# Optimization experiments

Measured on AMD Instinct MI355X. Metric: run time of the kernel, lower is better.

Reference implementation:

```python
import jax, jax.numpy as jnp
import numpy as np

LEAKY_SLOPE = 0.2  # PyG GATConv default negative_slope
EPS = 1e-16


def _gat_layer(h_in, src, dst, W, a_src, a_dst, b, concat):
    # h_in: [N, Fin]; src/dst: [Etot] (self-loops included); W: [Fin, H*C]
    N = h_in.shape[0]
    H, C = a_src.shape
    h = (h_in @ W).reshape(N, H, C)                       # [N,H,C]
    al_s = jnp.sum(h * a_src, axis=-1)                    # [N,H]
    al_d = jnp.sum(h * a_dst, axis=-1)                    # [N,H]
    e = jax.nn.leaky_relu(al_s[src] + al_d[dst], LEAKY_SLOPE)  # [E,H]
    emax = jax.ops.segment_max(e, dst, num_segments=N)    # segment softmax over dst
    p = jnp.exp(e - emax[dst])
    denom = jax.ops.segment_sum(p, dst, num_segments=N)
    alpha = p / (denom[dst] + EPS)                        # [E,H]
    out = jax.ops.segment_sum(h[src] * alpha[:, :, None], dst, num_segments=N)  # [N,H,C]
    out = out.reshape(N, H * C) if concat else out.mean(axis=1)
    return out + b


def setup_inputs() -> dict:
    key = jax.random.key(0)
    ks = jax.random.split(key, 16)
    N, E, Fin, Hd, Hh = 10000, 320000, 256, 128, 4

    def glorot(k, shape, fan_in):
        return jax.random.normal(k, shape, dtype=jnp.float32) * (1.0 / np.sqrt(fan_in))

    inp = {
        "x": jax.random.normal(ks[0], (N, Fin), dtype=jnp.float32),
        "edge_index": jax.random.randint(ks[1], (2, E), 0, N, dtype=jnp.int32),
        # conv1: Fin -> Hd x Hh heads, concat
        "W1": glorot(ks[2], (Fin, Hh * Hd), Fin),
        "a1_src": glorot(ks[3], (Hh, Hd), Hd),
        "a1_dst": glorot(ks[4], (Hh, Hd), Hd),
        "b1": jnp.zeros((Hh * Hd,), jnp.float32),
        # conv2: Hh*Hd -> Hd x Hh heads, concat
        "W2": glorot(ks[5], (Hh * Hd, Hh * Hd), Hh * Hd),
        "a2_src": glorot(ks[6], (Hh, Hd), Hd),
        "a2_dst": glorot(ks[7], (Hh, Hd), Hd),
        "b2": jnp.zeros((Hh * Hd,), jnp.float32),
        # conv3: Hh*Hd -> Hd, 1 head, concat=False (mean)
        "W3": glorot(ks[8], (Hh * Hd, Hd), Hh * Hd),
        "a3_src": glorot(ks[9], (1, Hd), Hd),
        "a3_dst": glorot(ks[10], (1, Hd), Hd),
        "b3": jnp.zeros((Hd,), jnp.float32),
        # classifier: Hd -> Hd//2 -> 2
        "Wc1": glorot(ks[11], (Hd, Hd // 2), Hd),
        "bc1": jnp.zeros((Hd // 2,), jnp.float32),
        "Wc2": glorot(ks[12], (Hd // 2, 2), Hd // 2),
        "bc2": jnp.zeros((2,), jnp.float32),
    }
    return inp


def reference(x, edge_index, W1, a1_src, a1_dst, b1, W2, a2_src, a2_dst, b2,
              W3, a3_src, a3_dst, b3, Wc1, bc1, Wc2, bc2):
    N = x.shape[0]
    loops = jnp.arange(N, dtype=edge_index.dtype)
    src = jnp.concatenate([edge_index[0], loops])  # PyG adds self-loops
    dst = jnp.concatenate([edge_index[1], loops])

    h = jax.nn.elu(_gat_layer(x, src, dst, W1, a1_src, a1_dst, b1, concat=True))
    h = jax.nn.elu(_gat_layer(h, src, dst, W2, a2_src, a2_dst, b2, concat=True))
    embeddings = _gat_layer(h, src, dst, W3, a3_src, a3_dst, b3, concat=False)  # [N, 128]
    out = jax.nn.relu(embeddings @ Wc1 + bc1) @ Wc2 + bc2  # [N, 2]
    return out, embeddings
```

## Files before the change

kernel.cpp:

```cpp
#include <hip/hip_runtime.h>
#include <cstddef>

#define LEAKY 0.2f
#define EPS_DEN 1e-16f

typedef short bf8_t __attribute__((ext_vector_type(8)));
typedef float f4_t __attribute__((ext_vector_type(4)));
typedef unsigned short us4_t __attribute__((ext_vector_type(4)));

__device__ __forceinline__ unsigned short f2bf(float f) {
    unsigned u = __float_as_uint(f);
    unsigned r = (u + 0x7fffu + ((u >> 16) & 1u)) >> 16;
    return (unsigned short)r;
}
__device__ __forceinline__ float bf2f(unsigned short h) {
    return __uint_as_float(((unsigned)h) << 16);
}

__global__ void hist_kernel(const int* __restrict__ dst, int* __restrict__ counts, int E) {
    int i = blockIdx.x * blockDim.x + threadIdx.x;
    if (i < E) atomicAdd(&counts[dst[i]], 1);
}

__global__ void scan1_kernel(int* __restrict__ cnt, int* __restrict__ bsum, int N) {
    __shared__ int s[256];
    int t = threadIdx.x;
    int i = blockIdx.x * 256 + t;
    int v = (i < N) ? cnt[i] : 0;
    s[t] = v;
    __syncthreads();
#pragma unroll
    for (int st = 1; st < 256; st <<= 1) {
        int add = (t >= st) ? s[t - st] : 0;
        __syncthreads();
        s[t] += add;
        __syncthreads();
    }
    if (i < N) cnt[i] = s[t] - v;
    if (t == 255) bsum[blockIdx.x] = s[255];
}

__global__ void scan2_kernel(int* __restrict__ bsum, int* __restrict__ offs, int NB, int N) {
    int t = threadIdx.x;
    int v = (t < NB) ? bsum[t] : 0;
    int inc = v;
#pragma unroll
    for (int off = 1; off < 64; off <<= 1) {
        int u = __shfl_up(inc, off);
        if (t >= off) inc += u;
    }
    if (t < NB) bsum[t] = inc - v;
    if (t == 63) offs[N] = inc;
}

__global__ void scan3_kernel(int* __restrict__ cnt, const int* __restrict__ bsum,
                             int* __restrict__ offs, int N) {
    int i = blockIdx.x * 256 + threadIdx.x;
    if (i < N) {
        int o = cnt[i] + bsum[blockIdx.x];
        offs[i] = o;
        cnt[i] = o;
    }
}

__global__ void scatter_kernel(const int* __restrict__ src, const int* __restrict__ dst,
                               int* __restrict__ cursor, int* __restrict__ csrc, int E) {
    int i = blockIdx.x * blockDim.x + threadIdx.x;
    if (i < E) {
        int d = dst[i];
        int pos = atomicAdd(&cursor[d], 1);
        csrc[pos] = src[i];
    }
}

__global__ void split_kernel(const float* __restrict__ in, unsigned short* __restrict__ hi,
                             unsigned short* __restrict__ lo, int len) {
    int i = blockIdx.x * blockDim.x + threadIdx.x;
    if (i >= len) return;
    float v = in[i];
    unsigned short h = f2bf(v);
    hi[i] = h;
    lo[i] = f2bf(v - bf2f(h));
}

__global__ void wsplit_kernel(const float* __restrict__ W, unsigned short* __restrict__ hi,
                              unsigned short* __restrict__ lo, int K, int N) {
    int idx = blockIdx.x * blockDim.x + threadIdx.x;
    if (idx >= K * N) return;
    int n = idx / K, k = idx % K;
    float v = W[(size_t)k * N + n];
    unsigned short h = f2bf(v);
    hi[idx] = h;
    lo[idx] = f2bf(v - bf2f(h));
}

__global__ __launch_bounds__(256) void mfma_gemm_kernel(
    const unsigned short* __restrict__ Ahi, const unsigned short* __restrict__ Alo,
    const unsigned short* __restrict__ BThi, const unsigned short* __restrict__ BTlo,
    float* __restrict__ C, int M, int N, int K) {
    constexpr int BK = 32;
    __shared__ __align__(16) unsigned short sA[64 * BK];
    __shared__ __align__(16) unsigned short sB[128 * BK];
    int t = threadIdx.x;
    int w = t >> 6, lane = t & 63;
    int quad = lane >> 4, low = lane & 15;
    int m0 = blockIdx.y * 64, n0 = blockIdx.x * 128;
    int wm = (w & 1) * 32, wn = (w >> 1) * 64;

    f4_t acc[2][4];
#pragma unroll
    for (int i = 0; i < 2; i++)
#pragma unroll
        for (int j = 0; j < 4; j++) acc[i][j] = (f4_t){0.f, 0.f, 0.f, 0.f};

    int srow = lane >> 2;
    int schunk = lane & 3;

    const unsigned short* Ap[3] = {Ahi, Ahi, Alo};
    const unsigned short* Bp[3] = {BThi, BTlo, BThi};

    for (int pass = 0; pass < 3; pass++) {
        const unsigned short* A = Ap[pass];
        const unsigned short* B = Bp[pass];
        for (int k0 = 0; k0 < K; k0 += BK) {
            __syncthreads();
            {
                int gm = m0 + w * 16 + srow;
                if (gm >= M) gm = M - 1;
                const void* g = (const void*)(A + (size_t)gm * K + k0 + schunk * 8);
                void* l = (void*)((char*)sA + (size_t)(w * 1024));
                __builtin_amdgcn_global_load_lds((const __attribute__((address_space(1))) void*)g,
                                                 (__attribute__((address_space(3))) void*)l, 16, 0, 0);
            }
#pragma unroll
            for (int inst = 0; inst < 2; inst++) {
                int gn = n0 + w * 32 + inst * 16 + srow;
                const void* g = (const void*)(B + (size_t)gn * K + k0 + schunk * 8);
                void* l = (void*)((char*)sB + (size_t)(w * 2048 + inst * 1024));
                __builtin_amdgcn_global_load_lds((const __attribute__((address_space(1))) void*)g,
                                                 (__attribute__((address_space(3))) void*)l, 16, 0, 0);
            }
            __syncthreads();

            bf8_t af[2], bf[4];
#pragma unroll
            for (int i = 0; i < 2; i++) {
                int row = wm + i * 16 + low;
                af[i] = *(const bf8_t*)&sA[row * BK + quad * 8];
            }
#pragma unroll
            for (int j = 0; j < 4; j++) {
                int row = wn + j * 16 + low;
                bf[j] = *(const bf8_t*)&sB[row * BK + quad * 8];
            }
#pragma unroll
            for (int i = 0; i < 2; i++)
#pragma unroll
                for (int j = 0; j < 4; j++)
                    acc[i][j] = __builtin_amdgcn_mfma_f32_16x16x32_bf16(af[i], bf[j], acc[i][j], 0, 0, 0);
        }
    }

#pragma unroll
    for (int i = 0; i < 2; i++) {
#pragma unroll
        for (int r = 0; r < 4; r++) {
            int gm = m0 + wm + i * 16 + quad * 4 + r;
            if (gm >= M) continue;
#pragma unroll
            for (int j = 0; j < 4; j++) {
                int gn = n0 + wn + j * 16 + low;
                C[(size_t)gm * N + gn] = acc[i][j][r];
            }
        }
    }
}

__global__ void al_h4_kernel(const float* __restrict__ h, const float* __restrict__ a_src,
                             const float* __restrict__ a_dst, float* __restrict__ als,
                             float* __restrict__ ald, int N) {
    int wave = threadIdx.x >> 6, lane = threadIdx.x & 63;
    int n = blockIdx.x * 4 + wave;
    if (n >= N) return;
    const float* row = h + (size_t)n * 512;
    float ps[4] = {0, 0, 0, 0}, pd[4] = {0, 0, 0, 0};
#pragma unroll
    for (int k = 0; k < 8; k++) {
        int f = k * 64 + lane;
        float v = row[f];
        ps[k >> 1] += v * a_src[f];
        pd[k >> 1] += v * a_dst[f];
    }
#pragma unroll
    for (int off = 32; off; off >>= 1) {
#pragma unroll
        for (int hd = 0; hd < 4; hd++) {
            ps[hd] += __shfl_down(ps[hd], off);
            pd[hd] += __shfl_down(pd[hd], off);
        }
    }
    if (lane == 0) {
#pragma unroll
        for (int hd = 0; hd < 4; hd++) {
            als[n * 4 + hd] = ps[hd];
            ald[n * 4 + hd] = pd[hd];
        }
    }
}

__global__ void al_h1_kernel(const float* __restrict__ h, const float* __restrict__ a_src,
                             const float* __restrict__ a_dst, float* __restrict__ als,
                             float* __restrict__ ald, int N) {
    int wave = threadIdx.x >> 6, lane = threadIdx.x & 63;
    int n = blockIdx.x * 4 + wave;
    if (n >= N) return;
    const float* row = h + (size_t)n * 128;
    float v0 = row[lane], v1 = row[lane + 64];
    float ps = v0 * a_src[lane] + v1 * a_src[lane + 64];
    float pd = v0 * a_dst[lane] + v1 * a_dst[lane + 64];
#pragma unroll
    for (int off = 32; off; off >>= 1) {
        ps += __shfl_down(ps, off);
        pd += __shfl_down(pd, off);
    }
    if (lane == 0) { als[n] = ps; ald[n] = pd; }
}

__global__ void stats_h4_kernel(const int* __restrict__ csrc, const int* __restrict__ offs,
                                const float* __restrict__ als, const float* __restrict__ ald,
                                float* __restrict__ pbuf, float* __restrict__ psf,
                                float* __restrict__ rden, int N, int E) {
    int wave = threadIdx.x >> 6, lane = threadIdx.x & 63;
    int n = blockIdx.x * 4 + wave;
    if (n >= N) return;
    int hd = lane & 3, es = lane >> 2;
    float aldn = ald[n * 4 + hd];
    float selfe = als[n * 4 + hd] + aldn;
    selfe = selfe > 0.f ? selfe : LEAKY * selfe;
    int beg = offs[n], end = offs[n + 1];
    float* pb = pbuf + (size_t)hd * E;
    float m = selfe;
    for (int base = beg; base + es < end; base += 16) {
        int idx = base + es;
        int s = csrc[idx];
        float e = als[s * 4 + hd] + aldn;
        e = e > 0.f ? e : LEAKY * e;
        pb[idx] = e;
        m = fmaxf(m, e);
    }
#pragma unroll
    for (int off = 4; off < 64; off <<= 1) m = fmaxf(m, __shfl_xor(m, off));
    float d = 0.f;
    for (int base = beg; base + es < end; base += 16) {
        int idx = base + es;
        float p = __expf(pb[idx] - m);
        pb[idx] = p;
        d += p;
    }
#pragma unroll
    for (int off = 4; off < 64; off <<= 1) d += __shfl_xor(d, off);
    float pself = __expf(selfe - m);
    float r = 1.0f / (d + pself + EPS_DEN);
    if (es == 0) {
        psf[n * 4 + hd] = pself;
        rden[n * 4 + hd] = r;
    }
}

__global__ void stats_h1_kernel(const int* __restrict__ csrc, const int* __restrict__ offs,
                                const float* __restrict__ als, const float* __restrict__ ald,
                                float* __restrict__ pbuf, float* __restrict__ psf,
                                float* __restrict__ rden, int N) {
    int wave = threadIdx.x >> 6, lane = threadIdx.x & 63;
    int n = blockIdx.x * 4 + wave;
    if (n >= N) return;
    float aldn = ald[n];
    float selfe = als[n] + aldn;
    selfe = selfe > 0.f ? selfe : LEAKY * selfe;
    int beg = offs[n], end = offs[n + 1];
    float m = selfe;
    for (int base = beg; base + lane < end; base += 64) {
        int idx = base + lane;
        int s = csrc[idx];
        float e = als[s] + aldn;
        e = e > 0.f ? e : LEAKY * e;
        pbuf[idx] = e;
        m = fmaxf(m, e);
    }
#pragma unroll
    for (int off = 1; off < 64; off <<= 1) m = fmaxf(m, __shfl_xor(m, off));
    float d = 0.f;
    for (int base = beg; base + lane < end; base += 64) {
        int idx = base + lane;
        float p = __expf(pbuf[idx] - m);
        pbuf[idx] = p;
        d += p;
    }
#pragma unroll
    for (int off = 1; off < 64; off <<= 1) d += __shfl_xor(d, off);
    float pself = __expf(selfe - m);
    float r = 1.0f / (d + pself + EPS_DEN);
    if (lane == 0) { psf[n] = pself; rden[n] = r; }
}

template <bool DO_ELU>
__global__ __launch_bounds__(64) void gat_aggregate_h4_kernel(
    const float* __restrict__ h, const float* __restrict__ pbuf,
    const float* __restrict__ psf, const float* __restrict__ rden,
    const int* __restrict__ csrc, const int* __restrict__ offs,
    const float* __restrict__ bias, unsigned short* __restrict__ ohi,
    unsigned short* __restrict__ olo, int N, int E) {
    int gid = blockIdx.x;
    int head = gid & 3;
    int n = gid >> 2;
    int lane = threadIdx.x;
    int half = lane >> 5;
    int fl = (lane & 31) * 4;
    int f0 = head * 128 + fl;
    const float* pb = pbuf + (size_t)head * E;
    f4_t acc;
    {
        float pself = (half == 0) ? psf[n * 4 + head] : 0.f;
        f4_t x = *(const f4_t*)(h + (size_t)n * 512 + f0);
        acc = pself * x;
    }
    __shared__ int sSrc[64];
    __shared__ float sP[64];
    int beg = offs[n], end = offs[n + 1];
    for (int base = beg; base < end; base += 64) {
        int len = min(64, end - base);
        __syncthreads();
        if (lane < len) {
            sSrc[lane] = csrc[base + lane];
            sP[lane] = pb[base + lane];
        }
        __syncthreads();
#pragma unroll 8
        for (int c = half; c < len; c += 2) {
            const float* srow = h + (size_t)sSrc[c] * 512;
            float p = sP[c];
            f4_t x = *(const f4_t*)(srow + f0);
            acc += p * x;
        }
    }
#pragma unroll
    for (int j = 0; j < 4; j++) acc[j] += __shfl_xor(acc[j], 32);
    float r = rden[n * 4 + head];
    f4_t b = *(const f4_t*)(bias + f0);
    us4_t hs, ls;
#pragma unroll
    for (int j = 0; j < 4; j++) {
        float o = acc[j] * r + b[j];
        if (DO_ELU) o = o > 0.f ? o : (__expf(o) - 1.0f);
        unsigned short hh = f2bf(o);
        hs[j] = hh;
        ls[j] = f2bf(o - bf2f(hh));
    }
    if (half == 0) {
        size_t idx = (size_t)n * 512 + f0;
        *(us4_t*)&ohi[idx] = hs;
        *(us4_t*)&olo[idx] = ls;
    }
}

__global__ __launch_bounds__(64) void gat_aggregate_h1_kernel(
    const float* __restrict__ h, const float* __restrict__ pbuf,
    const float* __restrict__ psf, const float* __restrict__ rden,
    const int* __restrict__ csrc, const int* __restrict__ offs,
    const float* __restrict__ bias, float* __restrict__ outp, int N) {
    int n = blockIdx.x;
    int lane = threadIdx.x;
    int half = lane >> 5;
    int f0 = (lane & 31) * 4;
    f4_t acc;
    {
        float pself = (half == 0) ? psf[n] : 0.f;
        f4_t x = *(const f4_t*)(h + (size_t)n * 128 + f0);
        acc = pself * x;
    }
    __shared__ int sSrc[64];
    __shared__ float sP[64];
    int beg = offs[n], end = offs[n + 1];
    for (int base = beg; base < end; base += 64) {
        int len = min(64, end - base);
        __syncthreads();
        if (lane < len) {
            sSrc[lane] = csrc[base + lane];
            sP[lane] = pbuf[base + lane];
        }
        __syncthreads();
#pragma unroll 8
        for (int c = half; c < len; c += 2) {
            const float* srow = h + (size_t)sSrc[c] * 128;
            float p = sP[c];
            f4_t x = *(const f4_t*)(srow + f0);
            acc += p * x;
        }
    }
#pragma unroll
    for (int j = 0; j < 4; j++) acc[j] += __shfl_xor(acc[j], 32);
    if (half == 0) {
        float r = rden[n];
        f4_t b = *(const f4_t*)(bias + f0);
        f4_t o;
#pragma unroll
        for (int j = 0; j < 4; j++) o[j] = acc[j] * r + b[j];
        *(f4_t*)&outp[(size_t)n * 128 + f0] = o;
    }
}

__global__ void classifier_kernel(const float* __restrict__ emb, const float* __restrict__ Wc1,
                                  const float* __restrict__ bc1, const float* __restrict__ Wc2,
                                  const float* __restrict__ bc2, float* __restrict__ out, int N) {
    int wave = threadIdx.x >> 6, lane = threadIdx.x & 63;
    int n = blockIdx.x * 4 + wave;
    if (n >= N) return;
    const float* row = emb + (size_t)n * 128;
    float acc = bc1[lane];
#pragma unroll 4
    for (int k = 0; k < 128; k++) acc += row[k] * Wc1[k * 64 + lane];
    acc = fmaxf(acc, 0.f);
    float o0 = acc * Wc2[lane * 2 + 0];
    float o1 = acc * Wc2[lane * 2 + 1];
#pragma unroll
    for (int off = 32; off; off >>= 1) {
        o0 += __shfl_down(o0, off);
        o1 += __shfl_down(o1, off);
    }
    if (lane == 0) {
        out[n * 2 + 0] = o0 + bc2[0];
        out[n * 2 + 1] = o1 + bc2[1];
    }
}

extern "C" void kernel_launch(void* const* d_in, const int* in_sizes, int n_in,
                              void* d_out, int out_size, void* d_ws, size_t ws_size,
                              hipStream_t stream) {
    const float* x      = (const float*)d_in[0];
    const int*   ei     = (const int*)d_in[1];
    const float* W1     = (const float*)d_in[2];
    const float* a1s    = (const float*)d_in[3];
    const float* a1d    = (const float*)d_in[4];
    const float* b1     = (const float*)d_in[5];
    const float* W2     = (const float*)d_in[6];
    const float* a2s    = (const float*)d_in[7];
    const float* a2d    = (const float*)d_in[8];
    const float* b2     = (const float*)d_in[9];
    const float* W3     = (const float*)d_in[10];
    const float* a3s    = (const float*)d_in[11];
    const float* a3d    = (const float*)d_in[12];
    const float* b3     = (const float*)d_in[13];
    const float* Wc1    = (const float*)d_in[14];
    const float* bc1    = (const float*)d_in[15];
    const float* Wc2    = (const float*)d_in[16];
    const float* bc2    = (const float*)d_in[17];

    const int N = in_sizes[0] / 256;
    const int E = in_sizes[1] / 2;
    const int F = 512;

    const int* src = ei;
    const int* dst = ei + E;

    auto align = [](size_t o) { return (o + 255) & ~(size_t)255; };
    size_t o = 0;
    size_t o_G     = o; o = align(o + (size_t)N * F * 4);
    size_t o_ahi   = o; o = align(o + (size_t)N * F * 2);
    size_t o_alo   = o; o = align(o + (size_t)N * F * 2);
    size_t o_xhi   = o; o = align(o + (size_t)N * 256 * 2);
    size_t o_xlo   = o; o = align(o + (size_t)N * 256 * 2);
    size_t o_w1h   = o; o = align(o + (size_t)512 * 256 * 2);
    size_t o_w1l   = o; o = align(o + (size_t)512 * 256 * 2);
    size_t o_w2h   = o; o = align(o + (size_t)512 * 512 * 2);
    size_t o_w2l   = o; o = align(o + (size_t)512 * 512 * 2);
    size_t o_w3h   = o; o = align(o + (size_t)128 * 512 * 2);
    size_t o_w3l   = o; o = align(o + (size_t)128 * 512 * 2);
    size_t o_als   = o; o = align(o + (size_t)N * 4 * 4);
    size_t o_ald   = o; o = align(o + (size_t)N * 4 * 4);
    size_t o_psf   = o; o = align(o + (size_t)N * 4 * 4);
    size_t o_rden  = o; o = align(o + (size_t)N * 4 * 4);
    size_t o_cnt   = o; o = align(o + (size_t)N * 4);
    size_t o_off   = o; o = align(o + (size_t)(N + 1) * 4);
    size_t o_bsum  = o; o = align(o + (size_t)64 * 4);
    size_t o_csrc  = o; o = align(o + (size_t)E * 4);
    size_t o_ebuf  = o; o = align(o + (size_t)E * 4 * 4);
    (void)ws_size;

    char* ws = (char*)d_ws;
    float* bufG  = (float*)(ws + o_G);
    unsigned short* act_hi = (unsigned short*)(ws + o_ahi);
    unsigned short* act_lo = (unsigned short*)(ws + o_alo);
    unsigned short* x_hi   = (unsigned short*)(ws + o_xhi);
    unsigned short* x_lo   = (unsigned short*)(ws + o_xlo);
    unsigned short* w1h = (unsigned short*)(ws + o_w1h);
    unsigned short* w1l = (unsigned short*)(ws + o_w1l);
    unsigned short* w2h = (unsigned short*)(ws + o_w2h);
    unsigned short* w2l = (unsigned short*)(ws + o_w2l);
    unsigned short* w3h = (unsigned short*)(ws + o_w3h);
    unsigned short* w3l = (unsigned short*)(ws + o_w3l);
    float* als  = (float*)(ws + o_als);
    float* ald  = (float*)(ws + o_ald);
    float* psf  = (float*)(ws + o_psf);
    float* rden = (float*)(ws + o_rden);
    int*   cnt  = (int*)(ws + o_cnt);
    int*   offs = (int*)(ws + o_off);
    int*   bsum = (int*)(ws + o_bsum);
    int*   csrc = (int*)(ws + o_csrc);
    float* ebuf = (float*)(ws + o_ebuf);

    float* outp = (float*)d_out;
    float* emb  = (float*)d_out + (size_t)N * 2;

    hipMemsetAsync(cnt, 0, (size_t)N * 4, stream);
    int eb = (E + 255) / 256;
    int nbs = (N + 255) / 256;
    hipLaunchKernelGGL(hist_kernel, dim3(eb), dim3(256), 0, stream, dst, cnt, E);
    hipLaunchKernelGGL(scan1_kernel, dim3(nbs), dim3(256), 0, stream, cnt, bsum, N);
    hipLaunchKernelGGL(scan2_kernel, dim3(1), dim3(64), 0, stream, bsum, offs, nbs, N);
    hipLaunchKernelGGL(scan3_kernel, dim3(nbs), dim3(256), 0, stream, cnt, bsum, offs, N);
    hipLaunchKernelGGL(scatter_kernel, dim3(eb), dim3(256), 0, stream, src, dst, cnt, csrc, E);

    hipLaunchKernelGGL(split_kernel, dim3((N * 256 + 255) / 256), dim3(256), 0, stream,
                       x, x_hi, x_lo, N * 256);
    hipLaunchKernelGGL(wsplit_kernel, dim3((256 * 512 + 255) / 256), dim3(256), 0, stream,
                       W1, w1h, w1l, 256, 512);
    hipLaunchKernelGGL(wsplit_kernel, dim3((512 * 512 + 255) / 256), dim3(256), 0, stream,
                       W2, w2h, w2l, 512, 512);
    hipLaunchKernelGGL(wsplit_kernel, dim3((512 * 128 + 255) / 256), dim3(256), 0, stream,
                       W3, w3h, w3l, 512, 128);

    int nb4 = (N + 3) / 4;
    int gy  = (N + 63) / 64;

    hipLaunchKernelGGL(mfma_gemm_kernel, dim3(512 / 128, gy), dim3(256), 0, stream,
                       x_hi, x_lo, w1h, w1l, bufG, N, 512, 256);
    hipLaunchKernelGGL(al_h4_kernel, dim3(nb4), dim3(256), 0, stream, bufG, a1s, a1d, als, ald, N);
    hipLaunchKernelGGL(stats_h4_kernel, dim3(nb4), dim3(256), 0, stream,
                       csrc, offs, als, ald, ebuf, psf, rden, N, E);
    hipLaunchKernelGGL((gat_aggregate_h4_kernel<true>), dim3(N * 4), dim3(64), 0, stream,
                       bufG, ebuf, psf, rden, csrc, offs, b1, act_hi, act_lo, N, E);

    hipLaunchKernelGGL(mfma_gemm_kernel, dim3(512 / 128, gy), dim3(256), 0, stream,
                       act_hi, act_lo, w2h, w2l, bufG, N, 512, 512);
    hipLaunchKernelGGL(al_h4_kernel, dim3(nb4), dim3(256), 0, stream, bufG, a2s, a2d, als, ald, N);
    hipLaunchKernelGGL(stats_h4_kernel, dim3(nb4), dim3(256), 0, stream,
                       csrc, offs, als, ald, ebuf, psf, rden, N, E);
    hipLaunchKernelGGL((gat_aggregate_h4_kernel<true>), dim3(N * 4), dim3(64), 0, stream,
                       bufG, ebuf, psf, rden, csrc, offs, b2, act_hi, act_lo, N, E);

    hipLaunchKernelGGL(mfma_gemm_kernel, dim3(128 / 128, gy), dim3(256), 0, stream,
                       act_hi, act_lo, w3h, w3l, bufG, N, 128, 512);
    hipLaunchKernelGGL(al_h1_kernel, dim3(nb4), dim3(256), 0, stream, bufG, a3s, a3d, als, ald, N);
    hipLaunchKernelGGL(stats_h1_kernel, dim3(nb4), dim3(256), 0, stream,
                       csrc, offs, als, ald, ebuf, psf, rden, N);
    hipLaunchKernelGGL(gat_aggregate_h1_kernel, dim3(N), dim3(64), 0, stream,
                       bufG, ebuf, psf, rden, csrc, offs, b3, emb, N);

    hipLaunchKernelGGL(classifier_kernel, dim3(nb4), dim3(256), 0, stream,
                       emb, Wc1, bc1, Wc2, bc2, outp, N);
}
```

Measured before the change: 397.4 us.

## Use 128x128 GEMM tiles, split aggregation per half-head, fuse classifier into final aggregate

Adds a 128x128-tile MFMA GEMM kernel for the two wide layers and keeps the 64x128 kernel for the narrow third layer. The intent is more data reuse per block and fewer blocks. The 4-head aggregation now launches 8 blocks per node, each covering a 64-feature slice with four edge groups, to raise parallelism on the gather. The classifier is fused into the final single-head aggregation, which removes one launch and a reread of the embeddings. The costs are more accumulator registers in the GEMM and each node's edge list being read twice as many times during aggregation.

```diff
diff --git a/kernel.cpp b/kernel.cpp
--- a/kernel.cpp
+++ b/kernel.cpp
@@ -94,7 +94,92 @@
     lo[idx] = f2bf(v - bf2f(h));
 }
 
-__global__ __launch_bounds__(256) void mfma_gemm_kernel(
+__global__ __launch_bounds__(256) void mfma_gemm128_kernel(
+    const unsigned short* __restrict__ Ahi, const unsigned short* __restrict__ Alo,
+    const unsigned short* __restrict__ BThi, const unsigned short* __restrict__ BTlo,
+    float* __restrict__ C, int M, int N, int K) {
+    constexpr int BK = 32;
+    __shared__ __align__(16) unsigned short sA[128 * BK];
+    __shared__ __align__(16) unsigned short sB[128 * BK];
+    int t = threadIdx.x;
+    int w = t >> 6, lane = t & 63;
+    int quad = lane >> 4, low = lane & 15;
+    int m0 = blockIdx.y * 128, n0 = blockIdx.x * 128;
+    int wm = (w & 1) * 64, wn = (w >> 1) * 64;
+
+    f4_t acc[4][4];
+#pragma unroll
+    for (int i = 0; i < 4; i++)
+#pragma unroll
+        for (int j = 0; j < 4; j++) acc[i][j] = (f4_t){0.f, 0.f, 0.f, 0.f};
+
+    int srow = lane >> 2;
+    int schunk = lane & 3;
+
+    const unsigned short* Ap[3] = {Ahi, Ahi, Alo};
+    const unsigned short* Bp[3] = {BThi, BTlo, BThi};
+
+    for (int pass = 0; pass < 3; pass++) {
+        const unsigned short* A = Ap[pass];
+        const unsigned short* B = Bp[pass];
+        for (int k0 = 0; k0 < K; k0 += BK) {
+            __syncthreads();
+#pragma unroll
+            for (int inst = 0; inst < 2; inst++) {
+                int r = w * 32 + inst * 16 + srow;
+                int gm = m0 + r;
+                if (gm >= M) gm = M - 1;
+                const void* g = (const void*)(A + (size_t)gm * K + k0 + schunk * 8);
+                void* l = (void*)((char*)sA + (size_t)(w * 2048 + inst * 1024));
+                __builtin_amdgcn_global_load_lds((const __attribute__((address_space(1))) void*)g,
+                                                 (__attribute__((address_space(3))) void*)l, 16, 0, 0);
+            }
+#pragma unroll
+            for (int inst = 0; inst < 2; inst++) {
+                int r = w * 32 + inst * 16 + srow;
+                int gn = n0 + r;
+                const void* g = (const void*)(B + (size_t)gn * K + k0 + schunk * 8);
+                void* l = (void*)((char*)sB + (size_t)(w * 2048 + inst * 1024));
+                __builtin_amdgcn_global_load_lds((const __attribute__((address_space(1))) void*)g,
+                                                 (__attribute__((address_space(3))) void*)l, 16, 0, 0);
+            }
+            __syncthreads();
+
+            bf8_t af[4], bf[4];
+#pragma unroll
+            for (int i = 0; i < 4; i++) {
+                int row = wm + i * 16 + low;
+                af[i] = *(const bf8_t*)&sA[row * BK + quad * 8];
+            }
+#pragma unroll
+            for (int j = 0; j < 4; j++) {
+                int row = wn + j * 16 + low;
+                bf[j] = *(const bf8_t*)&sB[row * BK + quad * 8];
+            }
+#pragma unroll
+            for (int i = 0; i < 4; i++)
+#pragma unroll
+                for (int j = 0; j < 4; j++)
+                    acc[i][j] = __builtin_amdgcn_mfma_f32_16x16x32_bf16(af[i], bf[j], acc[i][j], 0, 0, 0);
+        }
+    }
+
+#pragma unroll
+    for (int i = 0; i < 4; i++) {
+#pragma unroll
+        for (int r = 0; r < 4; r++) {
+            int gm = m0 + wm + i * 16 + quad * 4 + r;
+            if (gm >= M) continue;
+#pragma unroll
+            for (int j = 0; j < 4; j++) {
+                int gn = n0 + wn + j * 16 + low;
+                C[(size_t)gm * N + gn] = acc[i][j][r];
+            }
+        }
+    }
+}
+
+__global__ __launch_bounds__(256) void mfma_gemm64_kernel(
     const unsigned short* __restrict__ Ahi, const unsigned short* __restrict__ Alo,
     const unsigned short* __restrict__ BThi, const unsigned short* __restrict__ BTlo,
     float* __restrict__ C, int M, int N, int K) {
@@ -304,26 +389,22 @@
 }
 
 template <bool DO_ELU>
-__global__ __launch_bounds__(64) void gat_aggregate_h4_kernel(
+__global__ __launch_bounds__(64) void gat_agg_hh_kernel(
     const float* __restrict__ h, const float* __restrict__ pbuf,
     const float* __restrict__ psf, const float* __restrict__ rden,
     const int* __restrict__ csrc, const int* __restrict__ offs,
     const float* __restrict__ bias, unsigned short* __restrict__ ohi,
     unsigned short* __restrict__ olo, int N, int E) {
     int gid = blockIdx.x;
-    int head = gid & 3;
-    int n = gid >> 2;
+    int hh = gid & 7;
+    int n = gid >> 3;
+    int head = hh >> 1;
     int lane = threadIdx.x;
-    int half = lane >> 5;
-    int fl = (lane & 31) * 4;
-    int f0 = head * 128 + fl;
+    int eg = lane >> 4;
+    int f0 = hh * 64 + (lane & 15) * 4;
     const float* pb = pbuf + (size_t)head * E;
-    f4_t acc;
-    {
-        float pself = (half == 0) ? psf[n * 4 + head] : 0.f;
-        f4_t x = *(const f4_t*)(h + (size_t)n * 512 + f0);
-        acc = pself * x;
-    }
+
+    f4_t acc = (f4_t){0.f, 0.f, 0.f, 0.f};
     __shared__ int sSrc[64];
     __shared__ float sP[64];
     int beg = offs[n], end = offs[n + 1];
@@ -336,50 +417,56 @@
         }
         __syncthreads();
 #pragma unroll 8
-        for (int c = half; c < len; c += 2) {
+        for (int c = eg; c < len; c += 4) {
             const float* srow = h + (size_t)sSrc[c] * 512;
-            float p = sP[c];
             f4_t x = *(const f4_t*)(srow + f0);
-            acc += p * x;
-        }
-    }
-#pragma unroll
-    for (int j = 0; j < 4; j++) acc[j] += __shfl_xor(acc[j], 32);
-    float r = rden[n * 4 + head];
-    f4_t b = *(const f4_t*)(bias + f0);
-    us4_t hs, ls;
+            acc += sP[c] * x;
+        }
+    }
+    if (eg == 0) {
+        f4_t x = *(const f4_t*)(h + (size_t)n * 512 + f0);
+        acc += psf[n * 4 + head] * x;
+    }
 #pragma unroll
     for (int j = 0; j < 4; j++) {
-        float o = acc[j] * r + b[j];
-        if (DO_ELU) o = o > 0.f ? o : (__expf(o) - 1.0f);
-        unsigned short hh = f2bf(o);
-        hs[j] = hh;
-        ls[j] = f2bf(o - bf2f(hh));
-    }
-    if (half == 0) {
+        acc[j] += __shfl_xor(acc[j], 16);
+        acc[j] += __shfl_xor(acc[j], 32);
+    }
+    if (lane < 16) {
+        float r = rden[n * 4 + head];
+        f4_t b = *(const f4_t*)(bias + f0);
+        us4_t hs, ls;
+#pragma unroll
+        for (int j = 0; j < 4; j++) {
+            float o = acc[j] * r + b[j];
+            if (DO_ELU) o = o > 0.f ? o : (__expf(o) - 1.0f);
+            unsigned short hhh = f2bf(o);
+            hs[j] = hhh;
+            ls[j] = f2bf(o - bf2f(hhh));
+        }
         size_t idx = (size_t)n * 512 + f0;
         *(us4_t*)&ohi[idx] = hs;
         *(us4_t*)&olo[idx] = ls;
     }
 }
 
-__global__ __launch_bounds__(64) void gat_aggregate_h1_kernel(
+__global__ __launch_bounds__(64) void gat_agg_h1_cls_kernel(
     const float* __restrict__ h, const float* __restrict__ pbuf,
     const float* __restrict__ psf, const float* __restrict__ rden,
     const int* __restrict__ csrc, const int* __restrict__ offs,
-    const float* __restrict__ bias, float* __restrict__ outp, int N) {
+    const float* __restrict__ bias, const float* __restrict__ Wc1,
+    const float* __restrict__ bc1, const float* __restrict__ Wc2,
+    const float* __restrict__ bc2, float* __restrict__ emb,
+    float* __restrict__ outp, int N) {
     int n = blockIdx.x;
     int lane = threadIdx.x;
     int half = lane >> 5;
     int f0 = (lane & 31) * 4;
-    f4_t acc;
-    {
-        float pself = (half == 0) ? psf[n] : 0.f;
-        f4_t x = *(const f4_t*)(h + (size_t)n * 128 + f0);
-        acc = pself * x;
-    }
+
+    f4_t acc = (f4_t){0.f, 0.f, 0.f, 0.f};
     __shared__ int sSrc[64];
     __shared__ float sP[64];
+    __shared__ float semb[128];
     int beg = offs[n], end = offs[n + 1];
     for (int base = beg; base < end; base += 64) {
         int len = min(64, end - base);
@@ -392,44 +479,43 @@
 #pragma unroll 8
         for (int c = half; c < len; c += 2) {
             const float* srow = h + (size_t)sSrc[c] * 128;
-            float p = sP[c];
             f4_t x = *(const f4_t*)(srow + f0);
-            acc += p * x;
-        }
+            acc += sP[c] * x;
+        }
+    }
+    if (half == 0) {
+        f4_t x = *(const f4_t*)(h + (size_t)n * 128 + f0);
+        acc += psf[n] * x;
     }
 #pragma unroll
     for (int j = 0; j < 4; j++) acc[j] += __shfl_xor(acc[j], 32);
+
+    __syncthreads();
     if (half == 0) {
         float r = rden[n];
         f4_t b = *(const f4_t*)(bias + f0);
         f4_t o;
 #pragma unroll
         for (int j = 0; j < 4; j++) o[j] = acc[j] * r + b[j];
-        *(f4_t*)&outp[(size_t)n * 128 + f0] = o;
-    }
-}
-
-__global__ void classifier_kernel(const float* __restrict__ emb, const float* __restrict__ Wc1,
-                                  const float* __restrict__ bc1, const float* __restrict__ Wc2,
-                                  const float* __restrict__ bc2, float* __restrict__ out, int N) {
-    int wave = threadIdx.x >> 6, lane = threadIdx.x & 63;
-    int n = blockIdx.x * 4 + wave;
-    if (n >= N) return;
-    const float* row = emb + (size_t)n * 128;
-    float acc = bc1[lane];
+        *(f4_t*)&semb[f0] = o;
+        *(f4_t*)&emb[(size_t)n * 128 + f0] = o;
+    }
+    __syncthreads();
+
+    float cacc = bc1[lane];
 #pragma unroll 4
-    for (int k = 0; k < 128; k++) acc += row[k] * Wc1[k * 64 + lane];
-    acc = fmaxf(acc, 0.f);
-    float o0 = acc * Wc2[lane * 2 + 0];
-    float o1 = acc * Wc2[lane * 2 + 1];
+    for (int k = 0; k < 128; k++) cacc += semb[k] * Wc1[k * 64 + lane];
+    cacc = fmaxf(cacc, 0.f);
+    float o0 = cacc * Wc2[lane * 2 + 0];
+    float o1 = cacc * Wc2[lane * 2 + 1];
 #pragma unroll
     for (int off = 32; off; off >>= 1) {
         o0 += __shfl_down(o0, off);
         o1 += __shfl_down(o1, off);
     }
     if (lane == 0) {
-        out[n * 2 + 0] = o0 + bc2[0];
-        out[n * 2 + 1] = o1 + bc2[1];
+        outp[n * 2 + 0] = o0 + bc2[0];
+        outp[n * 2 + 1] = o1 + bc2[1];
     }
 }
 
@@ -530,32 +616,30 @@
                        W3, w3h, w3l, 512, 128);
 
     int nb4 = (N + 3) / 4;
-    int gy  = (N + 63) / 64;
-
-    hipLaunchKernelGGL(mfma_gemm_kernel, dim3(512 / 128, gy), dim3(256), 0, stream,
+    int gy128 = (N + 127) / 128;
+    int gy64  = (N + 63) / 64;
+
+    hipLaunchKernelGGL(mfma_gemm128_kernel, dim3(512 / 128, gy128), dim3(256), 0, stream,
                        x_hi, x_lo, w1h, w1l, bufG, N, 512, 256);
     hipLaunchKernelGGL(al_h4_kernel, dim3(nb4), dim3(256), 0, stream, bufG, a1s, a1d, als, ald, N);
     hipLaunchKernelGGL(stats_h4_kernel, dim3(nb4), dim3(256), 0, stream,
                        csrc, offs, als, ald, ebuf, psf, rden, N, E);
-    hipLaunchKernelGGL((gat_aggregate_h4_kernel<true>), dim3(N * 4), dim3(64), 0, stream,
+    hipLaunchKernelGGL((gat_agg_hh_kernel<true>), dim3(N * 8), dim3(64), 0, stream,
                        bufG, ebuf, psf, rden, csrc, offs, b1, act_hi, act_lo, N, E);
 
-    hipLaunchKernelGGL(mfma_gemm_kernel, dim3(512 / 128, gy), dim3(256), 0, stream,
+    hipLaunchKernelGGL(mfma_gemm128_kernel, dim3(512 / 128, gy128), dim3(256), 0, stream,
                        act_hi, act_lo, w2h, w2l, bufG, N, 512, 512);
     hipLaunchKernelGGL(al_h4_kernel, dim3(nb4), dim3(256), 0, stream, bufG, a2s, a2d, als, ald, N);
     hipLaunchKernelGGL(stats_h4_kernel, dim3(nb4), dim3(256), 0, stream,
                        csrc, offs, als, ald, ebuf, psf, rden, N, E);
-    hipLaunchKernelGGL((gat_aggregate_h4_kernel<true>), dim3(N * 4), dim3(64), 0, stream,
+    hipLaunchKernelGGL((gat_agg_hh_kernel<true>), dim3(N * 8), dim3(64), 0, stream,
                        bufG, ebuf, psf, rden, csrc, offs, b2, act_hi, act_lo, N, E);
 
-    hipLaunchKernelGGL(mfma_gemm_kernel, dim3(128 / 128, gy), dim3(256), 0, stream,
+    hipLaunchKernelGGL(mfma_gemm64_kernel, dim3(128 / 128, gy64), dim3(256), 0, stream,
                        act_hi, act_lo, w3h, w3l, bufG, N, 128, 512);
     hipLaunchKernelGGL(al_h1_kernel, dim3(nb4), dim3(256), 0, stream, bufG, a3s, a3d, als, ald, N);
     hipLaunchKernelGGL(stats_h1_kernel, dim3(nb4), dim3(256), 0, stream,
                        csrc, offs, als, ald, ebuf, psf, rden, N);
-    hipLaunchKernelGGL(gat_aggregate_h1_kernel, dim3(N), dim3(64), 0, stream,
-                       bufG, ebuf, psf, rden, csrc, offs, b3, emb, N);
-
-    hipLaunchKernelGGL(classifier_kernel, dim3(nb4), dim3(256), 0, stream,
-                       emb, Wc1, bc1, Wc2, bc2, outp, N);
-}
+    hipLaunchKernelGGL(gat_agg_h1_cls_kernel, dim3(N), dim3(64), 0, stream,
+                       bufG, ebuf, psf, rden, csrc, offs, b3, Wc1, bc1, Wc2, bc2, emb, outp, N);
+}
```

Result: no change. 391.7 us (-1.5%).
